# Performance work log

Hardware: AMD Instinct MI355X
Metric: run time of the kernel (lower is better)

Reference implementation:

```python
import jax, jax.numpy as jnp
import numpy as np

V, C, BLK = 32000, 512, 2048
B, T = 4, 2048
EPS = 1e-5


def _layernorm(x, g, b):
    mu = jnp.mean(x, axis=-1, keepdims=True)
    var = jnp.mean(jnp.square(x - mu), axis=-1, keepdims=True)
    return (x - mu) * jax.lax.rsqrt(var + EPS) * g + b


def setup_inputs() -> dict:
    key = jax.random.key(0)
    ks = jax.random.split(key, 16)
    s = 0.02
    return {
        "idx": jax.random.randint(ks[0], (B, T), 0, V),
        "targets": jax.random.randint(ks[1], (B, T), 0, V),
        "tok_emb": jax.random.normal(ks[2], (V, C), jnp.float32) * s,
        "pos_emb": jax.random.normal(ks[3], (BLK, C), jnp.float32) * s,
        "Wk": jax.random.normal(ks[4], (C, C), jnp.float32) * s,
        "Wq": jax.random.normal(ks[5], (C, C), jnp.float32) * s,
        "Wv": jax.random.normal(ks[6], (C, C), jnp.float32) * s,
        "W1": jax.random.normal(ks[7], (4 * C, C), jnp.float32) * s,
        "b1": jnp.zeros((4 * C,), jnp.float32),
        "W2": jax.random.normal(ks[8], (C, 4 * C), jnp.float32) * s,
        "b2": jnp.zeros((C,), jnp.float32),
        "g1": jnp.ones((C,), jnp.float32),
        "beta1": jnp.zeros((C,), jnp.float32),
        "g2": jnp.ones((C,), jnp.float32),
        "beta2": jnp.zeros((C,), jnp.float32),
        "Wlm": jax.random.normal(ks[9], (V, C), jnp.float32) * s,
        "blm": jnp.zeros((V,), jnp.float32),
    }


def reference(idx, targets, tok_emb, pos_emb, Wk, Wq, Wv, W1, b1, W2, b2,
              g1, beta1, g2, beta2, Wlm, blm):
    # embeddings
    x = tok_emb[idx] + pos_emb[:T]  # [B,T,C]
    # single-head causal self-attention (dropout = identity, eval mode)
    h = _layernorm(x, g1, beta1)
    q = jnp.einsum('btc,dc->btd', h, Wq)
    k = jnp.einsum('btc,dc->btd', h, Wk)
    v = jnp.einsum('btc,dc->btd', h, Wv)
    wei = jnp.einsum('btd,bsd->bts', q, k) * (C ** -0.5)  # [B,T,T]
    mask = jnp.tril(jnp.ones((T, T), bool))
    wei = jnp.where(mask, wei, -jnp.inf)
    wei = jax.nn.softmax(wei, axis=-1)
    x = x + jnp.einsum('bts,bsd->btd', wei, v)
    # FFN
    h2 = _layernorm(x, g2, beta2)
    ff = jax.nn.relu(jnp.einsum('btc,fc->btf', h2, W1) + b1)
    x = x + jnp.einsum('btf,cf->btc', ff, W2) + b2
    # lm head + cross-entropy
    logits = (jnp.einsum('btc,vc->btv', x, Wlm) + blm).reshape(B * T, V)
    logp = jax.nn.log_softmax(logits, axis=-1)
    loss = -jnp.mean(jnp.take_along_axis(logp, targets.reshape(-1, 1), axis=1))
    return logits, loss
```

## Files before the change

kernel.cpp:

```cpp
#include <hip/hip_runtime.h>

typedef __bf16 bf16;
typedef __bf16 bf16x8 __attribute__((ext_vector_type(8)));
typedef float  f32x4  __attribute__((ext_vector_type(4)));

#define NB 4
#define NT 2048
#define NC 512
#define NV 32000
#define NROWS (NB*NT)
#define NCHUNK (NV/256)
#define LNEPS 1e-5f
#define SMEM_B 131072

static __device__ __forceinline__ void load_lds16(const bf16* g, char* l) {
  __builtin_amdgcn_global_load_lds(
      (const __attribute__((address_space(1))) void*)g,
      (__attribute__((address_space(3))) void*)l, 16, 0, 0);
}

static __device__ __forceinline__ void bar() {
  asm volatile("" ::: "memory");
  __builtin_amdgcn_s_barrier();
  asm volatile("" ::: "memory");
}

__global__ __launch_bounds__(256)
void cvt_kernel(const float* __restrict__ in, bf16* __restrict__ out, int n8) {
  long i = (long)blockIdx.x * 256 + threadIdx.x;
  long stride = (long)gridDim.x * 256;
  for (; i < n8; i += stride) {
    const float* p = in + i * 8;
    f32x4 a = *(const f32x4*)p;
    f32x4 b = *(const f32x4*)(p + 4);
    bf16x8 o;
    o[0]=(bf16)a.x; o[1]=(bf16)a.y; o[2]=(bf16)a.z; o[3]=(bf16)a.w;
    o[4]=(bf16)b.x; o[5]=(bf16)b.y; o[6]=(bf16)b.z; o[7]=(bf16)b.w;
    *(bf16x8*)(out + i*8) = o;
  }
}

__global__ __launch_bounds__(64)
void embed_ln_kernel(const int* __restrict__ idx, const float* __restrict__ tok,
                     const float* __restrict__ pos, const float* __restrict__ gw,
                     const float* __restrict__ bw,
                     float* __restrict__ x0, bf16* __restrict__ h1) {
  int row = blockIdx.x;
  int t = row & (NT-1);
  int id = idx[row];
  int lane = threadIdx.x;
  const float* tr = tok + (long)id*NC + lane*8;
  const float* pr = pos + (long)t*NC + lane*8;
  f32x4 a0 = *(const f32x4*)tr, a1 = *(const f32x4*)(tr+4);
  f32x4 p0 = *(const f32x4*)pr, p1 = *(const f32x4*)(pr+4);
  f32x4 r0 = a0 + p0, r1 = a1 + p1;
  float* o = x0 + (long)row*NC + lane*8;
  *(f32x4*)o = r0; *(f32x4*)(o+4) = r1;
  float v[8] = {r0.x,r0.y,r0.z,r0.w,r1.x,r1.y,r1.z,r1.w};
  float s = 0.f;
  #pragma unroll
  for (int j=0;j<8;++j) s += v[j];
  #pragma unroll
  for (int m=32;m>=1;m>>=1) s += __shfl_xor(s, m);
  float mu = s * (1.f/NC);
  float sq = 0.f;
  #pragma unroll
  for (int j=0;j<8;++j) { v[j] -= mu; sq += v[j]*v[j]; }
  #pragma unroll
  for (int m=32;m>=1;m>>=1) sq += __shfl_xor(sq, m);
  float rs = rsqrtf(sq * (1.f/NC) + LNEPS);
  const float* gp = gw + lane*8;
  const float* bp = bw + lane*8;
  f32x4 g0 = *(const f32x4*)gp, g1 = *(const f32x4*)(gp+4);
  f32x4 b0 = *(const f32x4*)bp, b1 = *(const f32x4*)(bp+4);
  float gg[8] = {g0.x,g0.y,g0.z,g0.w,g1.x,g1.y,g1.z,g1.w};
  float bb[8] = {b0.x,b0.y,b0.z,b0.w,b1.x,b1.y,b1.z,b1.w};
  bf16x8 oo;
  #pragma unroll
  for (int j=0;j<8;++j) oo[j] = (bf16)(v[j]*rs*gg[j] + bb[j]);
  *(bf16x8*)(h1 + (long)row*NC + lane*8) = oo;
}

__global__ __launch_bounds__(64)
void ln_kernel(const float* __restrict__ x, const float* __restrict__ gw,
               const float* __restrict__ bw, bf16* __restrict__ out) {
  int row = blockIdx.x;
  int lane = threadIdx.x;
  const float* xr = x + (long)row*NC + lane*8;
  f32x4 a = *(const f32x4*)xr;
  f32x4 b = *(const f32x4*)(xr+4);
  float v[8] = {a.x,a.y,a.z,a.w,b.x,b.y,b.z,b.w};
  float s = 0.f;
  #pragma unroll
  for (int j=0;j<8;++j) s += v[j];
  #pragma unroll
  for (int m=32;m>=1;m>>=1) s += __shfl_xor(s, m);
  float mu = s * (1.f/NC);
  float sq = 0.f;
  #pragma unroll
  for (int j=0;j<8;++j) { v[j] -= mu; sq += v[j]*v[j]; }
  #pragma unroll
  for (int m=32;m>=1;m>>=1) sq += __shfl_xor(sq, m);
  float rs = rsqrtf(sq * (1.f/NC) + LNEPS);
  const float* gp = gw + lane*8;
  const float* bp = bw + lane*8;
  f32x4 g0 = *(const f32x4*)gp, g1 = *(const f32x4*)(gp+4);
  f32x4 b0 = *(const f32x4*)bp, b1 = *(const f32x4*)(bp+4);
  float gg[8] = {g0.x,g0.y,g0.z,g0.w,g1.x,g1.y,g1.z,g1.w};
  float bb[8] = {b0.x,b0.y,b0.z,b0.w,b1.x,b1.y,b1.z,b1.w};
  bf16x8 o;
  #pragma unroll
  for (int j=0;j<8;++j) o[j] = (bf16)(v[j]*rs*gg[j] + bb[j]);
  *(bf16x8*)(out + (long)row*NC + lane*8) = o;
}

__global__ __launch_bounds__(256)
void transpose_kernel(const bf16* __restrict__ v, long ldv, bf16* __restrict__ vt) {
  __shared__ bf16 tile[64][66];
  int b = blockIdx.z;
  int t0 = blockIdx.x*64, c0 = blockIdx.y*64;
  int tid = threadIdx.x;
  int r = tid >> 2, ch = (tid & 3) * 16;
  const bf16* src = v + ((long)b*NT + t0 + r)*ldv + c0 + ch;
  #pragma unroll
  for (int i=0;i<16;++i) tile[r][ch+i] = src[i];
  __syncthreads();
  bf16x8 o0, o1;
  #pragma unroll
  for (int i=0;i<8;++i) o0[i] = tile[ch+i][r];
  #pragma unroll
  for (int i=0;i<8;++i) o1[i] = tile[ch+8+i][r];
  bf16* dst = vt + ((long)b*NC + c0 + r)*NT + t0 + ch;
  *(bf16x8*)dst = o0;
  *(bf16x8*)(dst+8) = o1;
}

__global__ __launch_bounds__(256)
void softmax_kernel(float* __restrict__ S) {
  const int row = blockIdx.x;
  const int t = row & (NT-1);
  const int tid = threadIdx.x;
  float* sr = S + (long)row*NT;
  bf16* pr = (bf16*)S + (long)row*(2*NT);
  const float scale = 0.044194173824159216f;
  f32x4 v0 = *(const f32x4*)(sr + tid*8);
  f32x4 v1 = *(const f32x4*)(sr + tid*8 + 4);
  float v[8] = {v0.x,v0.y,v0.z,v0.w,v1.x,v1.y,v1.z,v1.w};
  int cb = tid*8;
  float mx = -1e30f;
  #pragma unroll
  for (int j=0;j<8;++j) {
    v[j] = (cb + j <= t) ? v[j]*scale : -1e30f;
    mx = fmaxf(mx, v[j]);
  }
  __shared__ float redm[4];
  #pragma unroll
  for (int m=32;m>=1;m>>=1) mx = fmaxf(mx, __shfl_xor(mx, m));
  if ((tid & 63) == 0) redm[tid>>6] = mx;
  __syncthreads();
  mx = fmaxf(fmaxf(redm[0],redm[1]), fmaxf(redm[2],redm[3]));
  float e[8]; float s = 0.f;
  #pragma unroll
  for (int j=0;j<8;++j) { e[j] = (cb + j <= t) ? __expf(v[j]-mx) : 0.f; s += e[j]; }
  __shared__ float reds[4];
  #pragma unroll
  for (int m=32;m>=1;m>>=1) s += __shfl_xor(s, m);
  if ((tid & 63) == 0) reds[tid>>6] = s;
  __syncthreads();
  s = reds[0]+reds[1]+reds[2]+reds[3];
  float inv = 1.f/s;
  bf16x8 o;
  #pragma unroll
  for (int j=0;j<8;++j) o[j] = (bf16)(e[j]*inv);
  *(bf16x8*)(pr + cb) = o;
}

enum { EPI_F32=0, EPI_BF16=1, EPI_BIAS_RELU_BF16=2, EPI_BIAS_RES_BF16=3, EPI_RES_F32=4, EPI_LMHEAD=5 };

template<int EPI, bool CAUSAL=false, bool KLIMIT=false, bool SWAP=false>
__global__ __launch_bounds__(512,2)
void gemm256(const bf16* __restrict__ A, const bf16* __restrict__ B, int nkt,
             long lda, long ldb, long sAb, long sBb,
             float* __restrict__ outf, bf16* __restrict__ outb, long ldo, long sOb,
             const float* __restrict__ bias,
             const float* __restrict__ res, long ldr, long sRb,
             float* __restrict__ pmax, float* __restrict__ psum) {
  extern __shared__ char smem[];
  int bn, bm;
  if constexpr (SWAP) { bm = blockIdx.x; bn = blockIdx.y; }
  else               { bn = blockIdx.x; bm = blockIdx.y; }
  const int bz = blockIdx.z;
  if constexpr (CAUSAL) { if (bn > bm) return; }
  int nkt_eff = nkt;
  if constexpr (KLIMIT) { int c = (bm+1)*4; if (c < nkt_eff) nkt_eff = c; }

  const int tid = threadIdx.x;
  const int wid = tid >> 6, lane = tid & 63;
  const int wr = wid >> 2, wc = wid & 3;
  const int l15 = lane & 15, g = lane >> 4;

  const bf16* Ab = A + (long)bz*sAb + (long)bm*256*lda;
  const bf16* Bb = B + (long)bz*sBb + (long)bn*256*ldb;

  const int colsw = 8 * ((tid & 7) ^ ((tid >> 3) & 7));
  const bf16* A0 = Ab + (long)(tid >> 3)*lda + colsw;
  const bf16* B0 = Bb + (long)(tid >> 3)*ldb + colsw;

  auto stage = [&](int ab, int t, int h, int slot) {
    char* dst = smem + slot*65536 + ab*32768 + h*16384 + wid*1024;
    const bf16* s0 = (ab ? B0 : A0) + (long)(h*128)*(ab ? ldb : lda) + (long)t*64;
    load_lds16(s0, dst);
    load_lds16(s0 + 64*(ab ? ldb : lda), dst + 8192);
  };

  const char* sm = smem;
  auto aLoad = [&](int slot, int m, int kk) -> bf16x8 {
    int row = m*16 + l15;
    int b = row*128 + ((kk*64 + g*16) ^ ((row & 7) << 4));
    return *(const bf16x8*)(sm + slot*65536 + wr*16384 + b);
  };
  auto bLoad = [&](int slot, int n, int kk) -> bf16x8 {
    int row = (wc & 1)*64 + n*16 + l15;
    int b = row*128 + ((kk*64 + g*16) ^ ((row & 7) << 4));
    return *(const bf16x8*)(sm + slot*65536 + 32768 + (wc >> 1)*16384 + b);
  };

  f32x4 acc[8][4] = {};

  stage(0, 0, 0, 0);
  stage(0, 0, 1, 0);
  stage(1, 0, 0, 0);
  stage(1, 0, 1, 0);
  stage(0, 1, 0, 1);
  asm volatile("s_waitcnt vmcnt(2)" ::: "memory");
  bar();

  const int niter = nkt_eff >> 1;
  for (int it = 0; it < niter; ++it) {
    const int t0 = 2*it, t1 = 2*it + 1;
    const int tn0 = (t0+2 < nkt_eff) ? t0+2 : nkt_eff-1;
    const int tn1 = (t1+2 < nkt_eff) ? t1+2 : nkt_eff-1;
    bf16x8 a0[4][2], a1[4][2], b0[2][2], b1[2][2];

    #pragma unroll
    for (int m=0;m<4;++m) { a0[m][0]=aLoad(0,m,0); a0[m][1]=aLoad(0,m,1); }
    #pragma unroll
    for (int n=0;n<2;++n) { b0[n][0]=bLoad(0,n,0); b0[n][1]=bLoad(0,n,1); }
    stage(0, t1, 1, 1);
    bar();
    __builtin_amdgcn_s_setprio(1);
    #pragma unroll
    for (int m=0;m<4;++m)
      #pragma unroll
      for (int n=0;n<2;++n) {
        acc[m][n] = __builtin_amdgcn_mfma_f32_16x16x32_bf16(a0[m][0], b0[n][0], acc[m][n],0,0,0);
        acc[m][n] = __builtin_amdgcn_mfma_f32_16x16x32_bf16(a0[m][1], b0[n][1], acc[m][n],0,0,0);
      }
    __builtin_amdgcn_s_setprio(0);
    bar();

    #pragma unroll
    for (int n=0;n<2;++n) { b1[n][0]=bLoad(0,n+2,0); b1[n][1]=bLoad(0,n+2,1); }
    stage(1, t1, 0, 1);
    bar();
    __builtin_amdgcn_s_setprio(1);
    #pragma unroll
    for (int m=0;m<4;++m)
      #pragma unroll
      for (int n=0;n<2;++n) {
        acc[m][n+2] = __builtin_amdgcn_mfma_f32_16x16x32_bf16(a0[m][0], b1[n][0], acc[m][n+2],0,0,0);
        acc[m][n+2] = __builtin_amdgcn_mfma_f32_16x16x32_bf16(a0[m][1], b1[n][1], acc[m][n+2],0,0,0);
      }
    __builtin_amdgcn_s_setprio(0);
    bar();

    #pragma unroll
    for (int m=0;m<4;++m) { a1[m][0]=aLoad(0,m+4,0); a1[m][1]=aLoad(0,m+4,1); }
    stage(1, t1, 1, 1);
    bar();
    __builtin_amdgcn_s_setprio(1);
    #pragma unroll
    for (int m=0;m<4;++m)
      #pragma unroll
      for (int n=0;n<2;++n) {
        acc[m+4][n+2] = __builtin_amdgcn_mfma_f32_16x16x32_bf16(a1[m][0], b1[n][0], acc[m+4][n+2],0,0,0);
        acc[m+4][n+2] = __builtin_amdgcn_mfma_f32_16x16x32_bf16(a1[m][1], b1[n][1], acc[m+4][n+2],0,0,0);
      }
    __builtin_amdgcn_s_setprio(0);
    bar();

    stage(0, tn0, 0, 0);
    asm volatile("s_waitcnt vmcnt(2)" ::: "memory");
    bar();
    __builtin_amdgcn_s_setprio(1);
    #pragma unroll
    for (int m=0;m<4;++m)
      #pragma unroll
      for (int n=0;n<2;++n) {
        acc[m+4][n] = __builtin_amdgcn_mfma_f32_16x16x32_bf16(a1[m][0], b0[n][0], acc[m+4][n],0,0,0);
        acc[m+4][n] = __builtin_amdgcn_mfma_f32_16x16x32_bf16(a1[m][1], b0[n][1], acc[m+4][n],0,0,0);
      }
    __builtin_amdgcn_s_setprio(0);
    bar();

    #pragma unroll
    for (int m=0;m<4;++m) { a0[m][0]=aLoad(1,m,0); a0[m][1]=aLoad(1,m,1); }
    #pragma unroll
    for (int n=0;n<2;++n) { b0[n][0]=bLoad(1,n,0); b0[n][1]=bLoad(1,n,1); }
    stage(0, tn0, 1, 0);
    bar();
    __builtin_amdgcn_s_setprio(1);
    #pragma unroll
    for (int m=0;m<4;++m)
      #pragma unroll
      for (int n=0;n<2;++n) {
        acc[m][n] = __builtin_amdgcn_mfma_f32_16x16x32_bf16(a0[m][0], b0[n][0], acc[m][n],0,0,0);
        acc[m][n] = __builtin_amdgcn_mfma_f32_16x16x32_bf16(a0[m][1], b0[n][1], acc[m][n],0,0,0);
      }
    __builtin_amdgcn_s_setprio(0);
    bar();

    #pragma unroll
    for (int n=0;n<2;++n) { b1[n][0]=bLoad(1,n+2,0); b1[n][1]=bLoad(1,n+2,1); }
    stage(1, tn0, 0, 0);
    bar();
    __builtin_amdgcn_s_setprio(1);
    #pragma unroll
    for (int m=0;m<4;++m)
      #pragma unroll
      for (int n=0;n<2;++n) {
        acc[m][n+2] = __builtin_amdgcn_mfma_f32_16x16x32_bf16(a0[m][0], b1[n][0], acc[m][n+2],0,0,0);
        acc[m][n+2] = __builtin_amdgcn_mfma_f32_16x16x32_bf16(a0[m][1], b1[n][1], acc[m][n+2],0,0,0);
      }
    __builtin_amdgcn_s_setprio(0);
    bar();

    #pragma unroll
    for (int m=0;m<4;++m) { a1[m][0]=aLoad(1,m+4,0); a1[m][1]=aLoad(1,m+4,1); }
    stage(1, tn0, 1, 0);
    bar();
    __builtin_amdgcn_s_setprio(1);
    #pragma unroll
    for (int m=0;m<4;++m)
      #pragma unroll
      for (int n=0;n<2;++n) {
        acc[m+4][n+2] = __builtin_amdgcn_mfma_f32_16x16x32_bf16(a1[m][0], b1[n][0], acc[m+4][n+2],0,0,0);
        acc[m+4][n+2] = __builtin_amdgcn_mfma_f32_16x16x32_bf16(a1[m][1], b1[n][1], acc[m+4][n+2],0,0,0);
      }
    __builtin_amdgcn_s_setprio(0);
    bar();

    stage(0, tn1, 0, 1);
    asm volatile("s_waitcnt vmcnt(2)" ::: "memory");
    bar();
    __builtin_amdgcn_s_setprio(1);
    #pragma unroll
    for (int m=0;m<4;++m)
      #pragma unroll
      for (int n=0;n<2;++n) {
        acc[m+4][n] = __builtin_amdgcn_mfma_f32_16x16x32_bf16(a1[m][0], b0[n][0], acc[m+4][n],0,0,0);
        acc[m+4][n] = __builtin_amdgcn_mfma_f32_16x16x32_bf16(a1[m][1], b0[n][1], acc[m+4][n],0,0,0);
      }
    __builtin_amdgcn_s_setprio(0);
    bar();
  }

  const long rowbase = (long)bm*256 + wr*128;
  const long colbase = (long)bn*256 + wc*64;

  if constexpr (EPI == EPI_LMHEAD) {
    #pragma unroll
    for (int m=0;m<8;++m)
      #pragma unroll
      for (int n=0;n<4;++n) {
        long c = colbase + n*16 + l15;
        float bv = bias[c];
        #pragma unroll
        for (int q_=0;q_<4;++q_) {
          acc[m][n][q_] += bv;
          long rr = rowbase + m*16 + g*4 + q_;
          __builtin_nontemporal_store(acc[m][n][q_], &outf[rr*ldo + c]);
        }
      }
    __syncthreads();
    float* redm = (float*)smem;
    float* reds = redm + 1024;
    #pragma unroll
    for (int m=0;m<8;++m)
      #pragma unroll
      for (int q_=0;q_<4;++q_) {
        float mx = fmaxf(fmaxf(acc[m][0][q_], acc[m][1][q_]),
                         fmaxf(acc[m][2][q_], acc[m][3][q_]));
        #pragma unroll
        for (int msk=8;msk>=1;msk>>=1) mx = fmaxf(mx, __shfl_xor(mx, msk));
        float se = 0.f;
        #pragma unroll
        for (int n=0;n<4;++n) se += __expf(acc[m][n][q_] - mx);
        #pragma unroll
        for (int msk=8;msk>=1;msk>>=1) se += __shfl_xor(se, msk);
        if (l15 == 0) {
          int rloc = wr*128 + m*16 + g*4 + q_;
          redm[wc*256 + rloc] = mx;
          reds[wc*256 + rloc] = se;
        }
      }
    __syncthreads();
    if (tid < 256) {
      float m0=redm[tid], m1=redm[256+tid], m2=redm[512+tid], m3=redm[768+tid];
      float M = fmaxf(fmaxf(m0,m1), fmaxf(m2,m3));
      float Sv = reds[tid]*__expf(m0-M) + reds[256+tid]*__expf(m1-M)
               + reds[512+tid]*__expf(m2-M) + reds[768+tid]*__expf(m3-M);
      long row = (long)bm*256 + tid;
      pmax[row*NCHUNK + bn] = M;
      psum[row*NCHUNK + bn] = Sv;
    }
  } else {
    #pragma unroll
    for (int m=0;m<8;++m)
      #pragma unroll
      for (int n=0;n<4;++n) {
        long c = colbase + n*16 + l15;
        #pragma unroll
        for (int q_=0;q_<4;++q_) {
          long rr = rowbase + m*16 + g*4 + q_;
          float v = acc[m][n][q_];
          if constexpr (EPI == EPI_F32) {
            outf[(long)bz*sOb + rr*ldo + c] = v;
          } else if constexpr (EPI == EPI_BF16) {
            outb[(long)bz*sOb + rr*ldo + c] = (bf16)v;
          } else if constexpr (EPI == EPI_BIAS_RELU_BF16) {
            outb[rr*ldo + c] = (bf16)fmaxf(v + bias[c], 0.f);
          } else if constexpr (EPI == EPI_BIAS_RES_BF16) {
            outb[rr*ldo + c] = (bf16)(v + bias[c] + res[rr*ldr + c]);
          } else if constexpr (EPI == EPI_RES_F32) {
            outf[(long)bz*sOb + rr*ldo + c] = v + res[(long)bz*sRb + rr*ldr + c];
          }
        }
      }
  }
}

__global__ __launch_bounds__(256)
void loss1_kernel(const float* __restrict__ pmax, const float* __restrict__ psum,
                  const float* __restrict__ logits, const int* __restrict__ targets,
                  float* __restrict__ rowloss) {
  int row = blockIdx.x;
  int tid = threadIdx.x;
  int lane = tid & 63, wv = tid >> 6;
  float cm = (tid < NCHUNK) ? pmax[(long)row*NCHUNK + tid] : -1e30f;
  float cs = (tid < NCHUNK) ? psum[(long)row*NCHUNK + tid] : 0.f;
  float mx = cm;
  #pragma unroll
  for (int m=32;m>=1;m>>=1) mx = fmaxf(mx, __shfl_xor(mx, m));
  __shared__ float rm[4];
  if (lane == 0) rm[wv] = mx;
  __syncthreads();
  float M = fmaxf(fmaxf(rm[0],rm[1]), fmaxf(rm[2],rm[3]));
  float sc = cs * __expf(cm - M);
  #pragma unroll
  for (int m=32;m>=1;m>>=1) sc += __shfl_xor(sc, m);
  __shared__ float rs_[4];
  if (lane == 0) rs_[wv] = sc;
  __syncthreads();
  if (tid == 0) {
    float Sv = rs_[0]+rs_[1]+rs_[2]+rs_[3];
    float lse = M + logf(Sv);
    int tgt = targets[row];
    float lg = logits[(long)row*NV + tgt];
    rowloss[row] = lse - lg;
  }
}

__global__ __launch_bounds__(256)
void loss2_kernel(const float* __restrict__ rowloss, float* __restrict__ out) {
  int tid = threadIdx.x;
  float s = 0.f;
  for (int i = tid; i < NROWS; i += 256) s += rowloss[i];
  #pragma unroll
  for (int m=32;m>=1;m>>=1) s += __shfl_xor(s, m);
  __shared__ float rs_[4];
  if ((tid & 63) == 0) rs_[tid>>6] = s;
  __syncthreads();
  if (tid == 0) out[0] = (rs_[0]+rs_[1]+rs_[2]+rs_[3]) * (1.f/NROWS);
}

extern "C" void kernel_launch(void* const* d_in, const int* in_sizes, int n_in,
                              void* d_out, int out_size, void* d_ws, size_t ws_size,
                              hipStream_t stream) {
  const int*   idx  = (const int*)d_in[0];
  const int*   tgt  = (const int*)d_in[1];
  const float* tok  = (const float*)d_in[2];
  const float* pos  = (const float*)d_in[3];
  const float* Wk   = (const float*)d_in[4];
  const float* Wq   = (const float*)d_in[5];
  const float* Wv   = (const float*)d_in[6];
  const float* W1   = (const float*)d_in[7];
  const float* b1   = (const float*)d_in[8];
  const float* W2   = (const float*)d_in[9];
  const float* b2   = (const float*)d_in[10];
  const float* g1   = (const float*)d_in[11];
  const float* be1  = (const float*)d_in[12];
  const float* g2   = (const float*)d_in[13];
  const float* be2  = (const float*)d_in[14];
  const float* Wlm  = (const float*)d_in[15];
  const float* blm  = (const float*)d_in[16];

  float* logits = (float*)d_out;
  float* loss   = logits + (long)NROWS*NV;

  char* w = (char*)d_ws;
  auto alloc = [&](size_t bytes) -> char* {
    char* p = w; w += (bytes + 255) & ~(size_t)255; return p;
  };
  bf16* wqkvb = (bf16*)alloc((size_t)3*NC*NC*2);
  bf16* w1b   = (bf16*)alloc((size_t)4*NC*NC*2);
  bf16* w2b   = (bf16*)alloc((size_t)4*NC*NC*2);
  bf16* wlmb  = (bf16*)alloc((size_t)NV*NC*2);
  float* x0   = (float*)alloc((size_t)NROWS*NC*4);
  bf16* h1b   = (bf16*)alloc((size_t)NROWS*NC*2);
  bf16* qkvb  = (bf16*)alloc((size_t)NROWS*3*NC*2);
  bf16* vtb   = (bf16*)alloc((size_t)NROWS*NC*2);
  float* Sb   = (float*)alloc((size_t)NB*NT*NT*4);
  float* x1   = (float*)alloc((size_t)NROWS*NC*4);
  bf16* h2b   = (bf16*)alloc((size_t)NROWS*NC*2);
  bf16* ffb   = (bf16*)alloc((size_t)NROWS*4*NC*2);
  bf16* x2b   = (bf16*)alloc((size_t)NROWS*NC*2);
  float* pmax = (float*)alloc((size_t)NROWS*NCHUNK*4);
  float* psum = (float*)alloc((size_t)NROWS*NCHUNK*4);
  float* rowloss = (float*)alloc((size_t)NROWS*4);

  hipFuncSetAttribute((const void*)gemm256<EPI_BF16,false,false,false>,
                      hipFuncAttributeMaxDynamicSharedMemorySize, SMEM_B);
  hipFuncSetAttribute((const void*)gemm256<EPI_F32,true,false,false>,
                      hipFuncAttributeMaxDynamicSharedMemorySize, SMEM_B);
  hipFuncSetAttribute((const void*)gemm256<EPI_RES_F32,false,true,false>,
                      hipFuncAttributeMaxDynamicSharedMemorySize, SMEM_B);
  hipFuncSetAttribute((const void*)gemm256<EPI_BIAS_RELU_BF16,false,false,true>,
                      hipFuncAttributeMaxDynamicSharedMemorySize, SMEM_B);
  hipFuncSetAttribute((const void*)gemm256<EPI_BIAS_RES_BF16,false,false,false>,
                      hipFuncAttributeMaxDynamicSharedMemorySize, SMEM_B);
  hipFuncSetAttribute((const void*)gemm256<EPI_LMHEAD,false,false,true>,
                      hipFuncAttributeMaxDynamicSharedMemorySize, SMEM_B);

  auto cvt = [&](const float* in, bf16* out, long n) {
    int n8 = (int)(n/8);
    int blocks = (n8 + 255)/256; if (blocks > 2048) blocks = 2048;
    cvt_kernel<<<blocks, 256, 0, stream>>>(in, out, n8);
  };
  cvt(Wq, wqkvb, (long)NC*NC);
  cvt(Wk, wqkvb + (long)NC*NC, (long)NC*NC);
  cvt(Wv, wqkvb + (long)2*NC*NC, (long)NC*NC);
  cvt(W1, w1b, (long)4*NC*NC);
  cvt(W2, w2b, (long)4*NC*NC);
  cvt(Wlm, wlmb, (long)NV*NC);

  embed_ln_kernel<<<NROWS, 64, 0, stream>>>(idx, tok, pos, g1, be1, x0, h1b);

  gemm256<EPI_BF16><<<dim3(6,32,1), 512, SMEM_B, stream>>>(
      h1b, wqkvb, 8, NC, NC, 0, 0, nullptr, qkvb, 3*NC, 0,
      nullptr, nullptr, 0, 0, nullptr, nullptr);

  transpose_kernel<<<dim3(NT/64, NC/64, NB), 256, 0, stream>>>(qkvb + 2*NC, 3*NC, vtb);

  gemm256<EPI_F32,true><<<dim3(8,8,NB), 512, SMEM_B, stream>>>(
      qkvb, qkvb + NC, 8, 3*NC, 3*NC, (long)NT*3*NC, (long)NT*3*NC,
      Sb, nullptr, NT, (long)NT*NT,
      nullptr, nullptr, 0, 0, nullptr, nullptr);

  softmax_kernel<<<NROWS, 256, 0, stream>>>(Sb);

  gemm256<EPI_RES_F32,false,true><<<dim3(2,8,NB), 512, SMEM_B, stream>>>(
      (const bf16*)Sb, vtb, 32, 2*NT, NT, (long)NT*2*NT, (long)NC*NT,
      x1, nullptr, NC, (long)NT*NC,
      nullptr, x0, NC, (long)NT*NC, nullptr, nullptr);

  ln_kernel<<<NROWS, 64, 0, stream>>>(x1, g2, be2, h2b);

  gemm256<EPI_BIAS_RELU_BF16,false,false,true><<<dim3(32,8,1), 512, SMEM_B, stream>>>(
      h2b, w1b, 8, NC, NC, 0, 0, nullptr, ffb, 4*NC, 0,
      b1, nullptr, 0, 0, nullptr, nullptr);

  gemm256<EPI_BIAS_RES_BF16><<<dim3(2,32,1), 512, SMEM_B, stream>>>(
      ffb, w2b, 32, 4*NC, 4*NC, 0, 0, nullptr, x2b, NC, 0,
      b2, x1, NC, 0, nullptr, nullptr);

  gemm256<EPI_LMHEAD,false,false,true><<<dim3(32,NCHUNK,1), 512, SMEM_B, stream>>>(
      x2b, wlmb, 8, NC, NC, 0, 0, logits, nullptr, NV, 0,
      blm, nullptr, 0, 0, pmax, psum);

  loss1_kernel<<<NROWS, 256, 0, stream>>>(pmax, psum, logits, tgt, rowloss);
  loss2_kernel<<<1, 256, 0, stream>>>(rowloss, loss);
}
```

Before: 774.1 us.

## Split-K the PV and FFN2 GEMMs, fuse combine+LN, add 128-tile LM head

```diff
diff --git a/kernel.cpp b/kernel.cpp
--- a/kernel.cpp
+++ b/kernel.cpp
@@ -9,7 +9,7 @@
 #define NC 512
 #define NV 32000
 #define NROWS (NB*NT)
-#define NCHUNK (NV/256)
+#define NCHUNK 250
 #define LNEPS 1e-5f
 #define SMEM_B 131072
 
@@ -81,39 +81,6 @@
   *(bf16x8*)(h1 + (long)row*NC + lane*8) = oo;
 }
 
-__global__ __launch_bounds__(64)
-void ln_kernel(const float* __restrict__ x, const float* __restrict__ gw,
-               const float* __restrict__ bw, bf16* __restrict__ out) {
-  int row = blockIdx.x;
-  int lane = threadIdx.x;
-  const float* xr = x + (long)row*NC + lane*8;
-  f32x4 a = *(const f32x4*)xr;
-  f32x4 b = *(const f32x4*)(xr+4);
-  float v[8] = {a.x,a.y,a.z,a.w,b.x,b.y,b.z,b.w};
-  float s = 0.f;
-  #pragma unroll
-  for (int j=0;j<8;++j) s += v[j];
-  #pragma unroll
-  for (int m=32;m>=1;m>>=1) s += __shfl_xor(s, m);
-  float mu = s * (1.f/NC);
-  float sq = 0.f;
-  #pragma unroll
-  for (int j=0;j<8;++j) { v[j] -= mu; sq += v[j]*v[j]; }
-  #pragma unroll
-  for (int m=32;m>=1;m>>=1) sq += __shfl_xor(sq, m);
-  float rs = rsqrtf(sq * (1.f/NC) + LNEPS);
-  const float* gp = gw + lane*8;
-  const float* bp = bw + lane*8;
-  f32x4 g0 = *(const f32x4*)gp, g1 = *(const f32x4*)(gp+4);
-  f32x4 b0 = *(const f32x4*)bp, b1 = *(const f32x4*)(bp+4);
-  float gg[8] = {g0.x,g0.y,g0.z,g0.w,g1.x,g1.y,g1.z,g1.w};
-  float bb[8] = {b0.x,b0.y,b0.z,b0.w,b1.x,b1.y,b1.z,b1.w};
-  bf16x8 o;
-  #pragma unroll
-  for (int j=0;j<8;++j) o[j] = (bf16)(v[j]*rs*gg[j] + bb[j]);
-  *(bf16x8*)(out + (long)row*NC + lane*8) = o;
-}
-
 __global__ __launch_bounds__(256)
 void transpose_kernel(const bf16* __restrict__ v, long ldv, bf16* __restrict__ vt) {
   __shared__ bf16 tile[64][66];
@@ -175,16 +142,15 @@
   *(bf16x8*)(pr + cb) = o;
 }
 
-enum { EPI_F32=0, EPI_BF16=1, EPI_BIAS_RELU_BF16=2, EPI_BIAS_RES_BF16=3, EPI_RES_F32=4, EPI_LMHEAD=5 };
-
-template<int EPI, bool CAUSAL=false, bool KLIMIT=false, bool SWAP=false>
+enum { EPI_F32=0, EPI_BF16=1, EPI_BIAS_RELU_BF16=2, EPI_BIAS_RES_BF16=3, EPI_RES_F32=4 };
+
+template<int EPI, bool CAUSAL=false, bool SWAP=false, bool KCHUNK=false>
 __global__ __launch_bounds__(512,2)
 void gemm256(const bf16* __restrict__ A, const bf16* __restrict__ B, int nkt,
              long lda, long ldb, long sAb, long sBb,
              float* __restrict__ outf, bf16* __restrict__ outb, long ldo, long sOb,
              const float* __restrict__ bias,
-             const float* __restrict__ res, long ldr, long sRb,
-             float* __restrict__ pmax, float* __restrict__ psum) {
+             const float* __restrict__ res, long ldr, long sRb) {
   extern __shared__ char smem[];
   int bn, bm;
   if constexpr (SWAP) { bm = blockIdx.x; bn = blockIdx.y; }
@@ -192,15 +158,23 @@
   const int bz = blockIdx.z;
   if constexpr (CAUSAL) { if (bn > bm) return; }
   int nkt_eff = nkt;
-  if constexpr (KLIMIT) { int c = (bm+1)*4; if (c < nkt_eff) nkt_eff = c; }
+  int bzAB = bz;
+  long kOff = 0;
+  if constexpr (KCHUNK) {
+    int c = bz >> 2; bzAB = bz & 3;
+    int lim = (bm+1)*4 - c*8;
+    if (lim <= 0) return;
+    if (lim < nkt_eff) nkt_eff = lim;
+    kOff = (long)c*512;
+  }
 
   const int tid = threadIdx.x;
   const int wid = tid >> 6, lane = tid & 63;
   const int wr = wid >> 2, wc = wid & 3;
   const int l15 = lane & 15, g = lane >> 4;
 
-  const bf16* Ab = A + (long)bz*sAb + (long)bm*256*lda;
-  const bf16* Bb = B + (long)bz*sBb + (long)bn*256*ldb;
+  const bf16* Ab = A + (long)bzAB*sAb + kOff + (long)bm*256*lda;
+  const bf16* Bb = B + (long)bzAB*sBb + kOff + (long)bn*256*ldb;
 
   const int colsw = 8 * ((tid & 7) ^ ((tid >> 3) & 7));
   const bf16* A0 = Ab + (long)(tid >> 3)*lda + colsw;
@@ -258,7 +232,6 @@
       }
     __builtin_amdgcn_s_setprio(0);
     bar();
-
     #pragma unroll
     for (int n=0;n<2;++n) { b1[n][0]=bLoad(0,n+2,0); b1[n][1]=bLoad(0,n+2,1); }
     stage(1, t1, 0, 1);
@@ -273,7 +246,6 @@
       }
     __builtin_amdgcn_s_setprio(0);
     bar();
-
     #pragma unroll
     for (int m=0;m<4;++m) { a1[m][0]=aLoad(0,m+4,0); a1[m][1]=aLoad(0,m+4,1); }
     stage(1, t1, 1, 1);
@@ -288,7 +260,6 @@
       }
     __builtin_amdgcn_s_setprio(0);
     bar();
-
     stage(0, tn0, 0, 0);
     asm volatile("s_waitcnt vmcnt(2)" ::: "memory");
     bar();
@@ -302,7 +273,6 @@
       }
     __builtin_amdgcn_s_setprio(0);
     bar();
-
     #pragma unroll
     for (int m=0;m<4;++m) { a0[m][0]=aLoad(1,m,0); a0[m][1]=aLoad(1,m,1); }
     #pragma unroll
@@ -319,7 +289,6 @@
       }
     __builtin_amdgcn_s_setprio(0);
     bar();
-
     #pragma unroll
     for (int n=0;n<2;++n) { b1[n][0]=bLoad(1,n+2,0); b1[n][1]=bLoad(1,n+2,1); }
     stage(1, tn0, 0, 0);
@@ -334,7 +303,6 @@
       }
     __builtin_amdgcn_s_setprio(0);
     bar();
-
     #pragma unroll
     for (int m=0;m<4;++m) { a1[m][0]=aLoad(1,m+4,0); a1[m][1]=aLoad(1,m+4,1); }
     stage(1, tn0, 1, 0);
@@ -349,7 +317,6 @@
       }
     __builtin_amdgcn_s_setprio(0);
     bar();
-
     stage(0, tn1, 0, 1);
     asm volatile("s_waitcnt vmcnt(2)" ::: "memory");
     bar();
@@ -368,76 +335,188 @@
   const long rowbase = (long)bm*256 + wr*128;
   const long colbase = (long)bn*256 + wc*64;
 
-  if constexpr (EPI == EPI_LMHEAD) {
-    #pragma unroll
-    for (int m=0;m<8;++m)
-      #pragma unroll
-      for (int n=0;n<4;++n) {
-        long c = colbase + n*16 + l15;
-        float bv = bias[c];
-        #pragma unroll
-        for (int q_=0;q_<4;++q_) {
-          acc[m][n][q_] += bv;
-          long rr = rowbase + m*16 + g*4 + q_;
-          __builtin_nontemporal_store(acc[m][n][q_], &outf[rr*ldo + c]);
+  #pragma unroll
+  for (int m=0;m<8;++m)
+    #pragma unroll
+    for (int n=0;n<4;++n) {
+      long c = colbase + n*16 + l15;
+      #pragma unroll
+      for (int q_=0;q_<4;++q_) {
+        long rr = rowbase + m*16 + g*4 + q_;
+        float v = acc[m][n][q_];
+        if constexpr (EPI == EPI_F32) {
+          outf[(long)bz*sOb + rr*ldo + c] = v;
+        } else if constexpr (EPI == EPI_BF16) {
+          outb[(long)bz*sOb + rr*ldo + c] = (bf16)v;
+        } else if constexpr (EPI == EPI_BIAS_RELU_BF16) {
+          outb[rr*ldo + c] = (bf16)fmaxf(v + bias[c], 0.f);
+        } else if constexpr (EPI == EPI_BIAS_RES_BF16) {
+          outb[rr*ldo + c] = (bf16)(v + bias[c] + res[rr*ldr + c]);
+        } else if constexpr (EPI == EPI_RES_F32) {
+          outf[(long)bz*sOb + rr*ldo + c] = v + res[(long)bz*sRb + rr*ldr + c];
         }
       }
+    }
+}
+
+__global__ __launch_bounds__(256)
+void lmhead128(const bf16* __restrict__ A, const bf16* __restrict__ B,
+               const float* __restrict__ bias, float* __restrict__ outf,
+               float* __restrict__ pmax, float* __restrict__ psum) {
+  __shared__ char As[8192];
+  __shared__ char Bs[8192];
+  const int bm = blockIdx.x, bn = blockIdx.y;
+  const int tid = threadIdx.x;
+  const int wid = tid >> 6, lane = tid & 63;
+  const int wr = wid >> 1, wc = wid & 1;
+  const int l15 = lane & 15, g = lane >> 4;
+
+  const int p0 = tid, p1 = tid + 256;
+  const int r0_ = 2*(p0>>3) + ((p0>>2)&1), c0_ = 8*((p0&3) ^ ((p0>>3)&3));
+  const int r1_ = 2*(p1>>3) + ((p1>>2)&1), c1_ = 8*((p1&3) ^ ((p1>>3)&3));
+  const bf16* A00 = A + ((long)bm*128 + r0_)*NC + c0_;
+  const bf16* A01 = A + ((long)bm*128 + r1_)*NC + c1_;
+  const bf16* B00 = B + ((long)bn*128 + r0_)*NC + c0_;
+  const bf16* B01 = B + ((long)bn*128 + r1_)*NC + c1_;
+  char* dA0 = As + wid*1024;
+  char* dA1 = As + 4096 + wid*1024;
+  char* dB0 = Bs + wid*1024;
+  char* dB1 = Bs + 4096 + wid*1024;
+
+  f32x4 acc[4][4] = {};
+
+  for (int kt = 0; kt < 16; ++kt) {
     __syncthreads();
-    float* redm = (float*)smem;
-    float* reds = redm + 1024;
-    #pragma unroll
-    for (int m=0;m<8;++m)
-      #pragma unroll
-      for (int q_=0;q_<4;++q_) {
-        float mx = fmaxf(fmaxf(acc[m][0][q_], acc[m][1][q_]),
-                         fmaxf(acc[m][2][q_], acc[m][3][q_]));
-        #pragma unroll
-        for (int msk=8;msk>=1;msk>>=1) mx = fmaxf(mx, __shfl_xor(mx, msk));
-        float se = 0.f;
-        #pragma unroll
-        for (int n=0;n<4;++n) se += __expf(acc[m][n][q_] - mx);
-        #pragma unroll
-        for (int msk=8;msk>=1;msk>>=1) se += __shfl_xor(se, msk);
-        if (l15 == 0) {
-          int rloc = wr*128 + m*16 + g*4 + q_;
-          redm[wc*256 + rloc] = mx;
-          reds[wc*256 + rloc] = se;
-        }
-      }
+    load_lds16(A00 + kt*32, dA0);
+    load_lds16(A01 + kt*32, dA1);
+    load_lds16(B00 + kt*32, dB0);
+    load_lds16(B01 + kt*32, dB1);
     __syncthreads();
-    if (tid < 256) {
-      float m0=redm[tid], m1=redm[256+tid], m2=redm[512+tid], m3=redm[768+tid];
-      float M = fmaxf(fmaxf(m0,m1), fmaxf(m2,m3));
-      float Sv = reds[tid]*__expf(m0-M) + reds[256+tid]*__expf(m1-M)
-               + reds[512+tid]*__expf(m2-M) + reds[768+tid]*__expf(m3-M);
-      long row = (long)bm*256 + tid;
-      pmax[row*NCHUNK + bn] = M;
-      psum[row*NCHUNK + bn] = Sv;
+    bf16x8 af[4], bf_[4];
+    #pragma unroll
+    for (int m=0;m<4;++m) {
+      int R = wr*64 + m*16 + l15;
+      af[m] = *(const bf16x8*)(As + (R>>1)*128 + (R&1)*64 + ((g ^ ((R>>1)&3))<<4));
     }
-  } else {
-    #pragma unroll
-    for (int m=0;m<8;++m)
-      #pragma unroll
-      for (int n=0;n<4;++n) {
-        long c = colbase + n*16 + l15;
-        #pragma unroll
-        for (int q_=0;q_<4;++q_) {
-          long rr = rowbase + m*16 + g*4 + q_;
-          float v = acc[m][n][q_];
-          if constexpr (EPI == EPI_F32) {
-            outf[(long)bz*sOb + rr*ldo + c] = v;
-          } else if constexpr (EPI == EPI_BF16) {
-            outb[(long)bz*sOb + rr*ldo + c] = (bf16)v;
-          } else if constexpr (EPI == EPI_BIAS_RELU_BF16) {
-            outb[rr*ldo + c] = (bf16)fmaxf(v + bias[c], 0.f);
-          } else if constexpr (EPI == EPI_BIAS_RES_BF16) {
-            outb[rr*ldo + c] = (bf16)(v + bias[c] + res[rr*ldr + c]);
-          } else if constexpr (EPI == EPI_RES_F32) {
-            outf[(long)bz*sOb + rr*ldo + c] = v + res[(long)bz*sRb + rr*ldr + c];
-          }
-        }
-      }
-  }
+    #pragma unroll
+    for (int n=0;n<4;++n) {
+      int R = wc*64 + n*16 + l15;
+      bf_[n] = *(const bf16x8*)(Bs + (R>>1)*128 + (R&1)*64 + ((g ^ ((R>>1)&3))<<4));
+    }
+    #pragma unroll
+    for (int m=0;m<4;++m)
+      #pragma unroll
+      for (int n=0;n<4;++n)
+        acc[m][n] = __builtin_amdgcn_mfma_f32_16x16x32_bf16(af[m], bf_[n], acc[m][n],0,0,0);
+  }
+
+  const long rowb = (long)bm*128;
+  const long colb = (long)bn*128;
+  #pragma unroll
+  for (int m=0;m<4;++m)
+    #pragma unroll
+    for (int n=0;n<4;++n) {
+      long c = colb + wc*64 + n*16 + l15;
+      float bv = bias[c];
+      #pragma unroll
+      for (int q=0;q<4;++q) {
+        acc[m][n][q] += bv;
+        long rr = rowb + wr*64 + m*16 + g*4 + q;
+        __builtin_nontemporal_store(acc[m][n][q], &outf[rr*NV + c]);
+      }
+    }
+  __syncthreads();
+  float* redm = (float*)As;
+  float* reds = redm + 256;
+  #pragma unroll
+  for (int m=0;m<4;++m)
+    #pragma unroll
+    for (int q=0;q<4;++q) {
+      float mx = fmaxf(fmaxf(acc[m][0][q], acc[m][1][q]),
+                       fmaxf(acc[m][2][q], acc[m][3][q]));
+      #pragma unroll
+      for (int msk=8;msk>=1;msk>>=1) mx = fmaxf(mx, __shfl_xor(mx, msk));
+      float se = 0.f;
+      #pragma unroll
+      for (int n=0;n<4;++n) se += __expf(acc[m][n][q] - mx);
+      #pragma unroll
+      for (int msk=8;msk>=1;msk>>=1) se += __shfl_xor(se, msk);
+      if (l15 == 0) {
+        int R = wr*64 + m*16 + g*4 + q;
+        redm[wc*128 + R] = mx;
+        reds[wc*128 + R] = se;
+      }
+    }
+  __syncthreads();
+  if (tid < 128) {
+    float m0 = redm[tid], m1 = redm[128+tid];
+    float M = fmaxf(m0, m1);
+    float Sv = reds[tid]*__expf(m0-M) + reds[128+tid]*__expf(m1-M);
+    long row = rowb + tid;
+    pmax[row*NCHUNK + bn] = M;
+    psum[row*NCHUNK + bn] = Sv;
+  }
+}
+
+__global__ __launch_bounds__(64)
+void pv_combine_ln_kernel(const float* __restrict__ part, const float* __restrict__ x0,
+                          const float* __restrict__ gw, const float* __restrict__ bw,
+                          float* __restrict__ x1, bf16* __restrict__ h2) {
+  int row = blockIdx.x;
+  int b = row >> 11, t = row & (NT-1);
+  int lane = threadIdx.x;
+  int nC = (t >> 9) + 1;
+  const float* xr = x0 + (long)row*NC + lane*8;
+  f32x4 a0 = *(const f32x4*)xr, a1 = *(const f32x4*)(xr+4);
+  for (int c = 0; c < nC; ++c) {
+    const float* pr = part + ((long)(c*4 + b)*NT + t)*NC + lane*8;
+    a0 += *(const f32x4*)pr; a1 += *(const f32x4*)(pr+4);
+  }
+  float* o = x1 + (long)row*NC + lane*8;
+  *(f32x4*)o = a0; *(f32x4*)(o+4) = a1;
+  float v[8] = {a0.x,a0.y,a0.z,a0.w,a1.x,a1.y,a1.z,a1.w};
+  float s = 0.f;
+  #pragma unroll
+  for (int j=0;j<8;++j) s += v[j];
+  #pragma unroll
+  for (int m=32;m>=1;m>>=1) s += __shfl_xor(s, m);
+  float mu = s * (1.f/NC);
+  float sq = 0.f;
+  #pragma unroll
+  for (int j=0;j<8;++j) { v[j] -= mu; sq += v[j]*v[j]; }
+  #pragma unroll
+  for (int m=32;m>=1;m>>=1) sq += __shfl_xor(sq, m);
+  float rs = rsqrtf(sq * (1.f/NC) + LNEPS);
+  const float* gp = gw + lane*8;
+  const float* bp = bw + lane*8;
+  f32x4 g0 = *(const f32x4*)gp, g1 = *(const f32x4*)(gp+4);
+  f32x4 b0 = *(const f32x4*)bp, b1 = *(const f32x4*)(bp+4);
+  float gg[8] = {g0.x,g0.y,g0.z,g0.w,g1.x,g1.y,g1.z,g1.w};
+  float bb[8] = {b0.x,b0.y,b0.z,b0.w,b1.x,b1.y,b1.z,b1.w};
+  bf16x8 oo;
+  #pragma unroll
+  for (int j=0;j<8;++j) oo[j] = (bf16)(v[j]*rs*gg[j] + bb[j]);
+  *(bf16x8*)(h2 + (long)row*NC + lane*8) = oo;
+}
+
+__global__ __launch_bounds__(64)
+void ffn2_combine_kernel(const float* __restrict__ part, const float* __restrict__ x1,
+                         const float* __restrict__ b2, bf16* __restrict__ x2) {
+  int row = blockIdx.x;
+  int lane = threadIdx.x;
+  const float* xr = x1 + (long)row*NC + lane*8;
+  f32x4 a0 = *(const f32x4*)xr, a1 = *(const f32x4*)(xr+4);
+  const float* br = b2 + lane*8;
+  a0 += *(const f32x4*)br; a1 += *(const f32x4*)(br+4);
+  #pragma unroll
+  for (int z = 0; z < 4; ++z) {
+    const float* pr = part + ((long)z*NROWS + row)*NC + lane*8;
+    a0 += *(const f32x4*)pr; a1 += *(const f32x4*)(pr+4);
+  }
+  bf16x8 o;
+  o[0]=(bf16)a0.x; o[1]=(bf16)a0.y; o[2]=(bf16)a0.z; o[3]=(bf16)a0.w;
+  o[4]=(bf16)a1.x; o[5]=(bf16)a1.y; o[6]=(bf16)a1.z; o[7]=(bf16)a1.w;
+  *(bf16x8*)(x2 + (long)row*NC + lane*8) = o;
 }
 
 __global__ __launch_bounds__(256)
@@ -521,6 +600,7 @@
   bf16* qkvb  = (bf16*)alloc((size_t)NROWS*3*NC*2);
   bf16* vtb   = (bf16*)alloc((size_t)NROWS*NC*2);
   float* Sb   = (float*)alloc((size_t)NB*NT*NT*4);
+  float* pvp  = (float*)alloc((size_t)16*NT*NC*4);
   float* x1   = (float*)alloc((size_t)NROWS*NC*4);
   bf16* h2b   = (bf16*)alloc((size_t)NROWS*NC*2);
   bf16* ffb   = (bf16*)alloc((size_t)NROWS*4*NC*2);
@@ -528,18 +608,17 @@
   float* pmax = (float*)alloc((size_t)NROWS*NCHUNK*4);
   float* psum = (float*)alloc((size_t)NROWS*NCHUNK*4);
   float* rowloss = (float*)alloc((size_t)NROWS*4);
+  float* ff2p = Sb;
 
   hipFuncSetAttribute((const void*)gemm256<EPI_BF16,false,false,false>,
                       hipFuncAttributeMaxDynamicSharedMemorySize, SMEM_B);
   hipFuncSetAttribute((const void*)gemm256<EPI_F32,true,false,false>,
                       hipFuncAttributeMaxDynamicSharedMemorySize, SMEM_B);
-  hipFuncSetAttribute((const void*)gemm256<EPI_RES_F32,false,true,false>,
+  hipFuncSetAttribute((const void*)gemm256<EPI_F32,false,false,true>,
                       hipFuncAttributeMaxDynamicSharedMemorySize, SMEM_B);
-  hipFuncSetAttribute((const void*)gemm256<EPI_BIAS_RELU_BF16,false,false,true>,
+  hipFuncSetAttribute((const void*)gemm256<EPI_F32,false,false,false>,
                       hipFuncAttributeMaxDynamicSharedMemorySize, SMEM_B);
-  hipFuncSetAttribute((const void*)gemm256<EPI_BIAS_RES_BF16,false,false,false>,
-                      hipFuncAttributeMaxDynamicSharedMemorySize, SMEM_B);
-  hipFuncSetAttribute((const void*)gemm256<EPI_LMHEAD,false,false,true>,
+  hipFuncSetAttribute((const void*)gemm256<EPI_BIAS_RELU_BF16,false,true,false>,
                       hipFuncAttributeMaxDynamicSharedMemorySize, SMEM_B);
 
   auto cvt = [&](const float* in, bf16* out, long n) {
@@ -558,35 +637,36 @@
 
   gemm256<EPI_BF16><<<dim3(6,32,1), 512, SMEM_B, stream>>>(
       h1b, wqkvb, 8, NC, NC, 0, 0, nullptr, qkvb, 3*NC, 0,
-      nullptr, nullptr, 0, 0, nullptr, nullptr);
+      nullptr, nullptr, 0, 0);
 
   transpose_kernel<<<dim3(NT/64, NC/64, NB), 256, 0, stream>>>(qkvb + 2*NC, 3*NC, vtb);
 
   gemm256<EPI_F32,true><<<dim3(8,8,NB), 512, SMEM_B, stream>>>(
       qkvb, qkvb + NC, 8, 3*NC, 3*NC, (long)NT*3*NC, (long)NT*3*NC,
       Sb, nullptr, NT, (long)NT*NT,
-      nullptr, nullptr, 0, 0, nullptr, nullptr);
+      nullptr, nullptr, 0, 0);
 
   softmax_kernel<<<NROWS, 256, 0, stream>>>(Sb);
 
-  gemm256<EPI_RES_F32,false,true><<<dim3(2,8,NB), 512, SMEM_B, stream>>>(
-      (const bf16*)Sb, vtb, 32, 2*NT, NT, (long)NT*2*NT, (long)NC*NT,
-      x1, nullptr, NC, (long)NT*NC,
-      nullptr, x0, NC, (long)NT*NC, nullptr, nullptr);
-
-  ln_kernel<<<NROWS, 64, 0, stream>>>(x1, g2, be2, h2b);
-
-  gemm256<EPI_BIAS_RELU_BF16,false,false,true><<<dim3(32,8,1), 512, SMEM_B, stream>>>(
+  gemm256<EPI_F32,false,false,true><<<dim3(2,8,16), 512, SMEM_B, stream>>>(
+      (const bf16*)Sb, vtb, 8, 2*NT, NT, (long)NT*2*NT, (long)NC*NT,
+      pvp, nullptr, NC, (long)NT*NC,
+      nullptr, nullptr, 0, 0);
+
+  pv_combine_ln_kernel<<<NROWS, 64, 0, stream>>>(pvp, x0, g2, be2, x1, h2b);
+
+  gemm256<EPI_BIAS_RELU_BF16,false,true><<<dim3(32,8,1), 512, SMEM_B, stream>>>(
       h2b, w1b, 8, NC, NC, 0, 0, nullptr, ffb, 4*NC, 0,
-      b1, nullptr, 0, 0, nullptr, nullptr);
-
-  gemm256<EPI_BIAS_RES_BF16><<<dim3(2,32,1), 512, SMEM_B, stream>>>(
-      ffb, w2b, 32, 4*NC, 4*NC, 0, 0, nullptr, x2b, NC, 0,
-      b2, x1, NC, 0, nullptr, nullptr);
-
-  gemm256<EPI_LMHEAD,false,false,true><<<dim3(32,NCHUNK,1), 512, SMEM_B, stream>>>(
-      x2b, wlmb, 8, NC, NC, 0, 0, logits, nullptr, NV, 0,
-      blm, nullptr, 0, 0, pmax, psum);
+      b1, nullptr, 0, 0);
+
+  gemm256<EPI_F32><<<dim3(2,32,4), 512, SMEM_B, stream>>>(
+      ffb, w2b, 8, 4*NC, 4*NC, 512, 512,
+      ff2p, nullptr, NC, (long)NROWS*NC,
+      nullptr, nullptr, 0, 0);
+
+  ffn2_combine_kernel<<<NROWS, 64, 0, stream>>>(ff2p, x1, b2, x2b);
+
+  lmhead128<<<dim3(64, NCHUNK), 256, 0, stream>>>(x2b, wlmb, blm, logits, pmax, psum);
 
   loss1_kernel<<<NROWS, 256, 0, stream>>>(pmax, psum, logits, tgt, rowloss);
   loss2_kernel<<<1, 256, 0, stream>>>(rowloss, loss);
```

Result: faster. 756.2 us (-2.3%).
